# Kernel optimization log

Hardware: AMD Instinct MI355X
Metric: run time of the kernel (lower is better)

Reference implementation:

```python
import jax, jax.numpy as jnp
import numpy as np

# init hyperparameters (from init_kwargs)
KD = KH = KW = 3
SD = SH = SW = 1
PD = PH = PW = 1
DD = DH = DW = 1
GROUPS = 1
DG = 1  # deformable_groups
CIN, COUT = 32, 64


def setup_inputs() -> dict:
    key = jax.random.key(0)
    k1, k2, k3, k4, k5 = jax.random.split(key, 5)
    B, D, H, W = 2, 8, 48, 48
    K = KD * KH * KW
    x = jax.random.normal(k1, (B, CIN, D, H, W), dtype=jnp.float32)
    # 2 offset components (h, w) per deformable-group kernel tap
    offset = jax.random.normal(k2, (B, 2 * DG * K, D, H, W), dtype=jnp.float32)
    mask = jax.random.uniform(k3, (B, DG * K, D, H, W), dtype=jnp.float32)
    fan_in = CIN // GROUPS * K
    weight = jax.random.normal(k4, (COUT, CIN // GROUPS, KD, KH, KW), dtype=jnp.float32) / np.sqrt(fan_in)
    bias = jax.random.uniform(k5, (COUT,), dtype=jnp.float32, minval=-1.0, maxval=1.0) / np.sqrt(fan_in)
    return {"input": x, "offset": offset, "mask": mask, "weight": weight, "bias": bias}


def reference(input, offset, mask, weight, bias):
    x = input
    B, Cin, D, H, W = x.shape
    Cout = weight.shape[0]
    K = KD * KH * KW
    Do = (D + 2 * PD - DD * (KD - 1) - 1) // SD + 1
    Ho = (H + 2 * PH - DH * (KH - 1) - 1) // SH + 1
    Wo = (W + 2 * PW - DW * (KW - 1) - 1) // SW + 1
    Cg = Cin // DG

    kdi, khi, kwi = [a.reshape(-1) for a in jnp.meshgrid(
        jnp.arange(KD), jnp.arange(KH), jnp.arange(KW), indexing="ij")]
    # depth taps: regular (un-deformed) dilated grid -> exact integer index
    d_pos = kdi[:, None] * DD + jnp.arange(Do) * SD - PD           # [K, Do]
    valid_d = (d_pos >= 0) & (d_pos < D)
    d_idx = jnp.clip(d_pos, 0, D - 1)
    h_base = (khi[:, None] * DH + jnp.arange(Ho) * SH - PH).astype(x.dtype)  # [K, Ho]
    w_base = (kwi[:, None] * DW + jnp.arange(Wo) * SW - PW).astype(x.dtype)  # [K, Wo]

    off = offset.reshape(B, DG, K, 2, Do, Ho, Wo)
    m = mask.reshape(B, DG, K, Do, Ho, Wo)

    h = h_base[None, None, :, None, :, None] + off[:, :, :, 0]     # [B,DG,K,Do,Ho,Wo]
    w = w_base[None, None, :, None, None, :] + off[:, :, :, 1]
    h0f, w0f = jnp.floor(h), jnp.floor(w)
    lh, lw = h - h0f, w - w0f
    h0, w0 = h0f.astype(jnp.int32), w0f.astype(jnp.int32)
    h1, w1 = h0 + 1, w0 + 1

    vd = valid_d[None, None, :, :, None, None]
    inb_h = lambda hi: (hi >= 0) & (hi < H)
    inb_w = lambda wi: (wi >= 0) & (wi < W)

    xg = x.reshape(B, DG, Cg, D, H, W)

    def gather(hI, wI):
        hc = jnp.clip(hI, 0, H - 1)
        wc = jnp.clip(wI, 0, W - 1)
        def per(xi, hh, ww):  # xi [Cg,D,H,W]; hh,ww [K,Do,Ho,Wo]
            dfull = jnp.broadcast_to(d_idx[:, :, None, None], hh.shape)
            return xi[:, dfull, hh, ww]  # [Cg,K,Do,Ho,Wo]
        return jax.vmap(jax.vmap(per))(xg, hc, wc)  # [B,DG,Cg,K,Do,Ho,Wo]

    w00 = ((1 - lh) * (1 - lw) * (inb_h(h0) & inb_w(w0) & vd))[:, :, None]
    w01 = ((1 - lh) * lw * (inb_h(h0) & inb_w(w1) & vd))[:, :, None]
    w10 = (lh * (1 - lw) * (inb_h(h1) & inb_w(w0) & vd))[:, :, None]
    w11 = (lh * lw * (inb_h(h1) & inb_w(w1) & vd))[:, :, None]

    val = (gather(h0, w0) * w00 + gather(h0, w1) * w01 +
           gather(h1, w0) * w10 + gather(h1, w1) * w11)   # [B,DG,Cg,K,Do,Ho,Wo]

    sampled = (val * m[:, :, None]).reshape(B, Cin, K, Do, Ho, Wo)
    w2 = weight.reshape(Cout, Cin // GROUPS, K)  # groups == 1
    out = jnp.einsum("bckdhw,ock->bodhw", sampled, w2)
    return out + bias[None, :, None, None, None]
```

## Files before the change

kernel.cpp:

```cpp
#include <hip/hip_runtime.h>
#include <hip/hip_fp16.h>

#define BSZ 2
#define CIN 32
#define COUT 64
#define DD_ 8
#define HH_ 48
#define WW_ 48
#define KK 27
#define HWs (HH_*WW_)
#define DHW (DD_*HH_*WW_)
#define NBLK (BSZ*DD_*HH_)

typedef __attribute__((ext_vector_type(8))) _Float16 half8;
typedef __attribute__((ext_vector_type(4))) float f32x4;

__device__ __forceinline__ half8 splat_h(unsigned packed, int hi) {
    union { unsigned v; _Float16 h[2]; } c; c.v = packed;
    _Float16 e = c.h[hi];
    return (half8){e, e, e, e, e, e, e, e};
}

__global__ void prep(const float* __restrict__ x, const float* __restrict__ wsrc,
                     _Float16* __restrict__ xT, _Float16* __restrict__ wf) {
    __shared__ float tile[CIN][WW_];
    int blk = blockIdx.x;
    if (blk < NBLK) {
        int h = blk % HH_;
        int t0 = blk / HH_;
        int d = t0 % DD_;
        int b = t0 / DD_;
        int base = d * HWs + h * WW_;
        for (int e = threadIdx.x; e < CIN * WW_; e += 256) {
            int ci = e / WW_, w = e - ci * WW_;
            tile[ci][w] = x[(size_t)(b * CIN + ci) * DHW + base + w];
        }
        __syncthreads();
        for (int e = threadIdx.x; e < CIN * WW_; e += 256) {
            int w = e >> 5, ci = e & 31;
            xT[(size_t)(b * DHW + base + w) * CIN + ci] = (_Float16)tile[ci][w];
        }
    } else {
        int idx = (blk - NBLK) * 256 + threadIdx.x;
        if (idx < KK * 4 * 64 * 8) {
            int j = idx & 7, l = (idx >> 3) & 63, c = (idx >> 9) & 3, k = idx >> 11;
            int co = c * 16 + (l & 15), ci = (l >> 4) * 8 + j;
            wf[idx] = (_Float16)wsrc[(co * CIN + ci) * KK + k];
        }
    }
}

__launch_bounds__(192, 3)
__global__ void dcn3d(const _Float16* __restrict__ xT,
                      const float* __restrict__ off, const float* __restrict__ msk,
                      const _Float16* __restrict__ wf,
                      const float* __restrict__ bias, float* __restrict__ out) {
    int blk = blockIdx.x;
    int h = blk % HH_;
    int t0 = blk / HH_;
    int d = t0 % DD_;
    int b = t0 / DD_;

    __shared__ uint4 Pp[KK * WW_];

    int tid = threadIdx.x;
    int lane = tid & 63;
    int T = tid >> 6;
    int wl = lane & 15;
    int g = lane >> 4;
    int spb = d * HWs + h * WW_;

    for (int p = tid; p < KK * WW_; p += 192) {
        int k = p / WW_;
        int w = p - k * WW_;
        int kd = k / 9, kh2 = (k / 3) % 3, kw2 = k % 3;
        int dpos = d + kd - 1;
        bool vd = (dpos >= 0) && (dpos < DD_);
        int didx = min(max(dpos, 0), DD_ - 1);
        int rb = didx * HWs;
        int sp = spb + w;
        float oh = off[(b * (2 * KK) + 2 * k) * DHW + sp];
        float ow = off[(b * (2 * KK) + 2 * k + 1) * DHW + sp];
        float m  = msk[(b * KK + k) * DHW + sp];
        float vm = vd ? m : 0.f;
        float hhf = (float)(kh2 + h - 1) + oh;
        float wwf = (float)(kw2 + w - 1) + ow;
        float h0f = floorf(hhf), w0f = floorf(wwf);
        float lh = hhf - h0f, lw = wwf - w0f;
        int h0 = (int)h0f, w0 = (int)w0f, h1 = h0 + 1, w1 = w0 + 1;
        bool ih0 = (h0 >= 0) && (h0 < HH_), ih1 = (h1 >= 0) && (h1 < HH_);
        bool iw0 = (w0 >= 0) && (w0 < WW_), iw1 = (w1 >= 0) && (w1 < WW_);
        int h0c = min(max(h0, 0), HH_ - 1), h1c = min(max(h1, 0), HH_ - 1);
        int w0c = min(max(w0, 0), WW_ - 1), w1c = min(max(w1, 0), WW_ - 1);
        float f00 = (ih0 && iw0) ? (1.f - lh) * (1.f - lw) * vm : 0.f;
        float f01 = (ih0 && iw1) ? (1.f - lh) * lw * vm : 0.f;
        float f10 = (ih1 && iw0) ? lh * (1.f - lw) * vm : 0.f;
        float f11 = (ih1 && iw1) ? lh * lw * vm : 0.f;
        uint4 P;
        P.x = (unsigned)(rb + h0c * WW_ + w0c) | ((unsigned)(rb + h0c * WW_ + w1c) << 16);
        P.y = (unsigned)(rb + h1c * WW_ + w0c) | ((unsigned)(rb + h1c * WW_ + w1c) << 16);
        __half2 ha = __floats2half2_rn(f00, f01);
        __half2 hb = __floats2half2_rn(f10, f11);
        P.z = *(const unsigned*)&ha;
        P.w = *(const unsigned*)&hb;
        Pp[p] = P;
    }
    __syncthreads();

    const _Float16* bp = xT + (size_t)b * DHW * CIN + g * 8;
    int pbase = T * 16 + wl;

    f32x4 acc0 = {0.f, 0.f, 0.f, 0.f};
    f32x4 acc1 = acc0, acc2 = acc0, acc3 = acc0;

    uint4 P0, P1, P2;
    half8 c0_00, c0_01, c0_10, c0_11;
    half8 c1_00, c1_01, c1_10, c1_11;
    half8 c2_00, c2_01, c2_10, c2_11;

#define PREAD(S, K) P##S = Pp[(K) * WW_ + pbase];
#define CISSUE(S) { \
    c##S##_00 = *(const half8*)(bp + ((size_t)(P##S.x & 0xFFFFu) << 5)); \
    c##S##_01 = *(const half8*)(bp + ((size_t)(P##S.x >> 16) << 5)); \
    c##S##_10 = *(const half8*)(bp + ((size_t)(P##S.y & 0xFFFFu) << 5)); \
    c##S##_11 = *(const half8*)(bp + ((size_t)(P##S.y >> 16) << 5)); }
#define COMP(S, K) { \
    const _Float16* wp = wf + (size_t)(K) * 2048 + lane * 8; \
    half8 a0 = *(const half8*)(wp); \
    half8 a1 = *(const half8*)(wp + 512); \
    half8 a2 = *(const half8*)(wp + 1024); \
    half8 a3 = *(const half8*)(wp + 1536); \
    half8 bf = c##S##_00 * splat_h(P##S.z, 0) + c##S##_01 * splat_h(P##S.z, 1) \
             + c##S##_10 * splat_h(P##S.w, 0) + c##S##_11 * splat_h(P##S.w, 1); \
    acc0 = __builtin_amdgcn_mfma_f32_16x16x32_f16(a0, bf, acc0, 0, 0, 0); \
    acc1 = __builtin_amdgcn_mfma_f32_16x16x32_f16(a1, bf, acc1, 0, 0, 0); \
    acc2 = __builtin_amdgcn_mfma_f32_16x16x32_f16(a2, bf, acc2, 0, 0, 0); \
    acc3 = __builtin_amdgcn_mfma_f32_16x16x32_f16(a3, bf, acc3, 0, 0, 0); }
#define STEP(J, CUR, NX2) CISSUE(NX2) COMP(CUR, J) PREAD(CUR, (J) + 3)

    PREAD(0, 0) PREAD(1, 1) PREAD(2, 2)
    CISSUE(0) CISSUE(1)

    STEP(0, 0, 2)  STEP(1, 1, 0)  STEP(2, 2, 1)
    STEP(3, 0, 2)  STEP(4, 1, 0)  STEP(5, 2, 1)
    STEP(6, 0, 2)  STEP(7, 1, 0)  STEP(8, 2, 1)
    STEP(9, 0, 2)  STEP(10, 1, 0) STEP(11, 2, 1)
    STEP(12, 0, 2) STEP(13, 1, 0) STEP(14, 2, 1)
    STEP(15, 0, 2) STEP(16, 1, 0) STEP(17, 2, 1)
    STEP(18, 0, 2) STEP(19, 1, 0) STEP(20, 2, 1)
    STEP(21, 0, 2) STEP(22, 1, 0) STEP(23, 2, 1)
    CISSUE(2) COMP(0, 24)
    COMP(1, 25)
    COMP(2, 26)

#undef PREAD
#undef CISSUE
#undef COMP
#undef STEP

    int rg = (lane >> 4) * 4;
    int wcol = T * 16 + (lane & 15);
    int obase = (b * COUT * DD_ + d) * HWs + h * WW_ + wcol;
#define ST(C, ACC)                                                         \
    _Pragma("unroll")                                                      \
    for (int r = 0; r < 4; ++r)                                            \
        out[obase + ((C) * 16 + rg + r) * DHW] = ACC[r] + bias[(C) * 16 + rg + r];
    ST(0, acc0) ST(1, acc1) ST(2, acc2) ST(3, acc3)
#undef ST
}

__global__ void dcn3d_ref(const float* __restrict__ x, const float* __restrict__ off,
                          const float* __restrict__ msk, const float* __restrict__ w,
                          const float* __restrict__ bias, float* __restrict__ out) {
    int blk = blockIdx.x;
    int h = blk % HH_;
    int t0 = blk / HH_;
    int d = t0 % DD_;
    int b = t0 / DD_;
    for (int e = threadIdx.x; e < COUT * WW_; e += 256) {
        int co = e / WW_, wo = e - co * WW_;
        float acc = bias[co];
        for (int k = 0; k < KK; ++k) {
            int kd = k / 9, kh2 = (k / 3) % 3, kw2 = k % 3;
            int dpos = d + kd - 1;
            if (dpos < 0 || dpos >= DD_) continue;
            int sp = d * HWs + h * WW_ + wo;
            float oh = off[(b * (2 * KK) + 2 * k) * DHW + sp];
            float ow = off[(b * (2 * KK) + 2 * k + 1) * DHW + sp];
            float m  = msk[(b * KK + k) * DHW + sp];
            float hhf = (float)(kh2 + h - 1) + oh;
            float wwf = (float)(kw2 + wo - 1) + ow;
            float h0f = floorf(hhf), w0f = floorf(wwf);
            float lh = hhf - h0f, lw = wwf - w0f;
            int h0 = (int)h0f, w0 = (int)w0f, h1 = h0 + 1, w1 = w0 + 1;
            bool ih0 = (h0 >= 0) && (h0 < HH_), ih1 = (h1 >= 0) && (h1 < HH_);
            bool iw0 = (w0 >= 0) && (w0 < WW_), iw1 = (w1 >= 0) && (w1 < WW_);
            int h0c = min(max(h0, 0), HH_ - 1), h1c = min(max(h1, 0), HH_ - 1);
            int w0c = min(max(w0, 0), WW_ - 1), w1c = min(max(w1, 0), WW_ - 1);
            float f00 = (ih0 && iw0) ? (1.f - lh) * (1.f - lw) * m : 0.f;
            float f01 = (ih0 && iw1) ? (1.f - lh) * lw * m : 0.f;
            float f10 = (ih1 && iw0) ? lh * (1.f - lw) * m : 0.f;
            float f11 = (ih1 && iw1) ? lh * lw * m : 0.f;
            int rb = dpos * HWs;
            for (int ci = 0; ci < CIN; ++ci) {
                const float* xp = x + (size_t)(b * CIN + ci) * DHW;
                float v = f00 * xp[rb + h0c * WW_ + w0c] + f01 * xp[rb + h0c * WW_ + w1c]
                        + f10 * xp[rb + h1c * WW_ + w0c] + f11 * xp[rb + h1c * WW_ + w1c];
                acc += w[(co * CIN + ci) * KK + k] * v;
            }
        }
        out[((b * COUT + co) * DD_ + d) * HWs + h * WW_ + wo] = acc;
    }
}

extern "C" void kernel_launch(void* const* d_in, const int* in_sizes, int n_in,
                              void* d_out, int out_size, void* d_ws, size_t ws_size,
                              hipStream_t stream) {
    const float* x    = (const float*)d_in[0];
    const float* off  = (const float*)d_in[1];
    const float* msk  = (const float*)d_in[2];
    const float* w    = (const float*)d_in[3];
    const float* bias = (const float*)d_in[4];
    float* out = (float*)d_out;

    const size_t XT_OFF   = 131072;
    const size_t XT_BYTES = (size_t)BSZ * DHW * CIN * sizeof(_Float16);

    _Float16* wf = (_Float16*)d_ws;
    _Float16* xT = (_Float16*)((char*)d_ws + XT_OFF);
    int use = (ws_size >= XT_OFF + XT_BYTES) ? 1 : 0;

    if (use) {
        int wblocks = (KK * 4 * 64 * 8 + 255) / 256;
        prep<<<NBLK + wblocks, 256, 0, stream>>>(x, w, xT, wf);
        dcn3d<<<NBLK, 192, 0, stream>>>(xT, off, msk, wf, bias, out);
    } else {
        dcn3d_ref<<<NBLK, 256, 0, stream>>>(x, off, msk, w, bias, out);
    }
}
```

Before: 42.76 us.

## Split kernel taps across waves with LDS atomic reduction and triple block count

Each block now handles 16 output columns instead of 48, and its four waves split the 27 kernel taps (padded to 28 with zero weights) rather than splitting the output columns. Partial MFMA accumulators are summed through shared-memory atomics before the store. This triples the grid and shortens each wave's serial tap chain to raise occupancy and hide gather latency. In exchange it adds LDS atomic traffic, an extra barrier, and a zero-padded tap.

```diff
diff --git a/kernel.cpp b/kernel.cpp
--- a/kernel.cpp
+++ b/kernel.cpp
@@ -11,6 +11,7 @@
 #define HWs (HH_*WW_)
 #define DHW (DD_*HH_*WW_)
 #define NBLK (BSZ*DD_*HH_)
+#define NTH 256
 
 typedef __attribute__((ext_vector_type(8))) _Float16 half8;
 typedef __attribute__((ext_vector_type(4))) float f32x4;
@@ -42,131 +43,146 @@
         }
     } else {
         int idx = (blk - NBLK) * 256 + threadIdx.x;
-        if (idx < KK * 4 * 64 * 8) {
+        if (idx < 28 * 4 * 64 * 8) {
             int j = idx & 7, l = (idx >> 3) & 63, c = (idx >> 9) & 3, k = idx >> 11;
             int co = c * 16 + (l & 15), ci = (l >> 4) * 8 + j;
-            wf[idx] = (_Float16)wsrc[(co * CIN + ci) * KK + k];
-        }
-    }
-}
-
-__launch_bounds__(192, 3)
+            wf[idx] = (k < KK) ? (_Float16)wsrc[(co * CIN + ci) * KK + k] : (_Float16)0.f;
+        }
+    }
+}
+
+__launch_bounds__(NTH, 5)
 __global__ void dcn3d(const _Float16* __restrict__ xT,
                       const float* __restrict__ off, const float* __restrict__ msk,
                       const _Float16* __restrict__ wf,
                       const float* __restrict__ bias, float* __restrict__ out) {
     int blk = blockIdx.x;
-    int h = blk % HH_;
-    int t0 = blk / HH_;
+    int T = blk % 3;
+    int row = blk / 3;
+    int h = row % HH_;
+    int t0 = row / HH_;
     int d = t0 % DD_;
     int b = t0 / DD_;
-
-    __shared__ uint4 Pp[KK * WW_];
+    int T16 = T * 16;
+
+    __shared__ uint4 Pp[28 * 16];
+    __shared__ float Cred[COUT * 17];
 
     int tid = threadIdx.x;
     int lane = tid & 63;
-    int T = tid >> 6;
+    int q = tid >> 6;
     int wl = lane & 15;
     int g = lane >> 4;
     int spb = d * HWs + h * WW_;
 
-    for (int p = tid; p < KK * WW_; p += 192) {
-        int k = p / WW_;
-        int w = p - k * WW_;
-        int kd = k / 9, kh2 = (k / 3) % 3, kw2 = k % 3;
-        int dpos = d + kd - 1;
-        bool vd = (dpos >= 0) && (dpos < DD_);
-        int didx = min(max(dpos, 0), DD_ - 1);
-        int rb = didx * HWs;
-        int sp = spb + w;
-        float oh = off[(b * (2 * KK) + 2 * k) * DHW + sp];
-        float ow = off[(b * (2 * KK) + 2 * k + 1) * DHW + sp];
-        float m  = msk[(b * KK + k) * DHW + sp];
-        float vm = vd ? m : 0.f;
-        float hhf = (float)(kh2 + h - 1) + oh;
-        float wwf = (float)(kw2 + w - 1) + ow;
-        float h0f = floorf(hhf), w0f = floorf(wwf);
-        float lh = hhf - h0f, lw = wwf - w0f;
-        int h0 = (int)h0f, w0 = (int)w0f, h1 = h0 + 1, w1 = w0 + 1;
-        bool ih0 = (h0 >= 0) && (h0 < HH_), ih1 = (h1 >= 0) && (h1 < HH_);
-        bool iw0 = (w0 >= 0) && (w0 < WW_), iw1 = (w1 >= 0) && (w1 < WW_);
-        int h0c = min(max(h0, 0), HH_ - 1), h1c = min(max(h1, 0), HH_ - 1);
-        int w0c = min(max(w0, 0), WW_ - 1), w1c = min(max(w1, 0), WW_ - 1);
-        float f00 = (ih0 && iw0) ? (1.f - lh) * (1.f - lw) * vm : 0.f;
-        float f01 = (ih0 && iw1) ? (1.f - lh) * lw * vm : 0.f;
-        float f10 = (ih1 && iw0) ? lh * (1.f - lw) * vm : 0.f;
-        float f11 = (ih1 && iw1) ? lh * lw * vm : 0.f;
-        uint4 P;
-        P.x = (unsigned)(rb + h0c * WW_ + w0c) | ((unsigned)(rb + h0c * WW_ + w1c) << 16);
-        P.y = (unsigned)(rb + h1c * WW_ + w0c) | ((unsigned)(rb + h1c * WW_ + w1c) << 16);
-        __half2 ha = __floats2half2_rn(f00, f01);
-        __half2 hb = __floats2half2_rn(f10, f11);
-        P.z = *(const unsigned*)&ha;
-        P.w = *(const unsigned*)&hb;
-        Pp[p] = P;
-    }
+    for (int e = tid; e < COUT * 17; e += NTH) Cred[e] = 0.f;
+
+#define PARAM(PIDX)                                                            \
+    {                                                                          \
+        int p = (PIDX);                                                        \
+        int k = p >> 4;                                                        \
+        uint4 P;                                                               \
+        if (k < KK) {                                                          \
+            int w = T16 + (p & 15);                                            \
+            int kd = k / 9, kh2 = (k / 3) % 3, kw2 = k % 3;                    \
+            int dpos = d + kd - 1;                                             \
+            bool vd = (dpos >= 0) && (dpos < DD_);                             \
+            int didx = min(max(dpos, 0), DD_ - 1);                             \
+            int rb = didx * HWs;                                               \
+            int sp = spb + w;                                                  \
+            float oh = off[(b * (2 * KK) + 2 * k) * DHW + sp];                 \
+            float ow = off[(b * (2 * KK) + 2 * k + 1) * DHW + sp];             \
+            float m  = msk[(b * KK + k) * DHW + sp];                           \
+            float vm = vd ? m : 0.f;                                           \
+            float hhf = (float)(kh2 + h - 1) + oh;                             \
+            float wwf = (float)(kw2 + w - 1) + ow;                             \
+            float h0f = floorf(hhf), w0f = floorf(wwf);                        \
+            float lh = hhf - h0f, lw = wwf - w0f;                              \
+            int h0 = (int)h0f, w0 = (int)w0f, h1 = h0 + 1, w1 = w0 + 1;        \
+            bool ih0 = (h0 >= 0) && (h0 < HH_), ih1 = (h1 >= 0) && (h1 < HH_); \
+            bool iw0 = (w0 >= 0) && (w0 < WW_), iw1 = (w1 >= 0) && (w1 < WW_); \
+            int h0c = min(max(h0, 0), HH_ - 1), h1c = min(max(h1, 0), HH_ - 1);\
+            int w0c = min(max(w0, 0), WW_ - 1), w1c = min(max(w1, 0), WW_ - 1);\
+            float f00 = (ih0 && iw0) ? (1.f - lh) * (1.f - lw) * vm : 0.f;     \
+            float f01 = (ih0 && iw1) ? (1.f - lh) * lw * vm : 0.f;             \
+            float f10 = (ih1 && iw0) ? lh * (1.f - lw) * vm : 0.f;             \
+            float f11 = (ih1 && iw1) ? lh * lw * vm : 0.f;                     \
+            P.x = (unsigned)(rb + h0c * WW_ + w0c)                             \
+                | ((unsigned)(rb + h0c * WW_ + w1c) << 16);                    \
+            P.y = (unsigned)(rb + h1c * WW_ + w0c)                             \
+                | ((unsigned)(rb + h1c * WW_ + w1c) << 16);                    \
+            __half2 ha = __floats2half2_rn(f00, f01);                          \
+            __half2 hb = __floats2half2_rn(f10, f11);                          \
+            P.z = *(const unsigned*)&ha;                                       \
+            P.w = *(const unsigned*)&hb;                                       \
+        } else {                                                               \
+            P.x = 0u; P.y = 0u; P.z = 0u; P.w = 0u;                            \
+        }                                                                      \
+        Pp[p] = P;                                                             \
+    }
+
+    PARAM(tid)
+    if (tid < 192) PARAM(tid + 256)
+#undef PARAM
     __syncthreads();
 
     const _Float16* bp = xT + (size_t)b * DHW * CIN + g * 8;
-    int pbase = T * 16 + wl;
 
     f32x4 acc0 = {0.f, 0.f, 0.f, 0.f};
     f32x4 acc1 = acc0, acc2 = acc0, acc3 = acc0;
 
-    uint4 P0, P1, P2;
-    half8 c0_00, c0_01, c0_10, c0_11;
-    half8 c1_00, c1_01, c1_10, c1_11;
-    half8 c2_00, c2_01, c2_10, c2_11;
-
-#define PREAD(S, K) P##S = Pp[(K) * WW_ + pbase];
-#define CISSUE(S) { \
-    c##S##_00 = *(const half8*)(bp + ((size_t)(P##S.x & 0xFFFFu) << 5)); \
-    c##S##_01 = *(const half8*)(bp + ((size_t)(P##S.x >> 16) << 5)); \
-    c##S##_10 = *(const half8*)(bp + ((size_t)(P##S.y & 0xFFFFu) << 5)); \
-    c##S##_11 = *(const half8*)(bp + ((size_t)(P##S.y >> 16) << 5)); }
-#define COMP(S, K) { \
-    const _Float16* wp = wf + (size_t)(K) * 2048 + lane * 8; \
+    uint4 PA, PB;
+    int kA, kB;
+    half8 cA00, cA01, cA10, cA11;
+    half8 cB00, cB01, cB10, cB11;
+
+#define PRD(S, I) { k##S = q + 4 * (I); P##S = Pp[(k##S << 4) + wl]; }
+#define ISS(S) { \
+    c##S##00 = *(const half8*)(bp + ((size_t)(P##S.x & 0xFFFFu) << 5)); \
+    c##S##01 = *(const half8*)(bp + ((size_t)(P##S.x >> 16) << 5)); \
+    c##S##10 = *(const half8*)(bp + ((size_t)(P##S.y & 0xFFFFu) << 5)); \
+    c##S##11 = *(const half8*)(bp + ((size_t)(P##S.y >> 16) << 5)); }
+#define CMP(S) { \
+    const _Float16* wp = wf + (size_t)k##S * 2048 + lane * 8; \
     half8 a0 = *(const half8*)(wp); \
     half8 a1 = *(const half8*)(wp + 512); \
     half8 a2 = *(const half8*)(wp + 1024); \
     half8 a3 = *(const half8*)(wp + 1536); \
-    half8 bf = c##S##_00 * splat_h(P##S.z, 0) + c##S##_01 * splat_h(P##S.z, 1) \
-             + c##S##_10 * splat_h(P##S.w, 0) + c##S##_11 * splat_h(P##S.w, 1); \
+    half8 bf = c##S##00 * splat_h(P##S.z, 0) + c##S##01 * splat_h(P##S.z, 1) \
+             + c##S##10 * splat_h(P##S.w, 0) + c##S##11 * splat_h(P##S.w, 1); \
     acc0 = __builtin_amdgcn_mfma_f32_16x16x32_f16(a0, bf, acc0, 0, 0, 0); \
     acc1 = __builtin_amdgcn_mfma_f32_16x16x32_f16(a1, bf, acc1, 0, 0, 0); \
     acc2 = __builtin_amdgcn_mfma_f32_16x16x32_f16(a2, bf, acc2, 0, 0, 0); \
     acc3 = __builtin_amdgcn_mfma_f32_16x16x32_f16(a3, bf, acc3, 0, 0, 0); }
-#define STEP(J, CUR, NX2) CISSUE(NX2) COMP(CUR, J) PREAD(CUR, (J) + 3)
-
-    PREAD(0, 0) PREAD(1, 1) PREAD(2, 2)
-    CISSUE(0) CISSUE(1)
-
-    STEP(0, 0, 2)  STEP(1, 1, 0)  STEP(2, 2, 1)
-    STEP(3, 0, 2)  STEP(4, 1, 0)  STEP(5, 2, 1)
-    STEP(6, 0, 2)  STEP(7, 1, 0)  STEP(8, 2, 1)
-    STEP(9, 0, 2)  STEP(10, 1, 0) STEP(11, 2, 1)
-    STEP(12, 0, 2) STEP(13, 1, 0) STEP(14, 2, 1)
-    STEP(15, 0, 2) STEP(16, 1, 0) STEP(17, 2, 1)
-    STEP(18, 0, 2) STEP(19, 1, 0) STEP(20, 2, 1)
-    STEP(21, 0, 2) STEP(22, 1, 0) STEP(23, 2, 1)
-    CISSUE(2) COMP(0, 24)
-    COMP(1, 25)
-    COMP(2, 26)
-
-#undef PREAD
-#undef CISSUE
-#undef COMP
-#undef STEP
-
-    int rg = (lane >> 4) * 4;
-    int wcol = T * 16 + (lane & 15);
-    int obase = (b * COUT * DD_ + d) * HWs + h * WW_ + wcol;
-#define ST(C, ACC)                                                         \
-    _Pragma("unroll")                                                      \
-    for (int r = 0; r < 4; ++r)                                            \
-        out[obase + ((C) * 16 + rg + r) * DHW] = ACC[r] + bias[(C) * 16 + rg + r];
-    ST(0, acc0) ST(1, acc1) ST(2, acc2) ST(3, acc3)
-#undef ST
+
+    PRD(A, 0) ISS(A)
+    PRD(B, 1) ISS(B)
+    CMP(A) PRD(A, 2) ISS(A)
+    CMP(B) PRD(B, 3) ISS(B)
+    CMP(A) PRD(A, 4) ISS(A)
+    CMP(B) PRD(B, 5) ISS(B)
+    CMP(A) PRD(A, 6) ISS(A)
+    CMP(B)
+    CMP(A)
+
+#undef PRD
+#undef ISS
+#undef CMP
+
+    int rg = g * 4;
+#define RED(C, ACC)                                                            \
+    _Pragma("unroll")                                                          \
+    for (int r = 0; r < 4; ++r)                                                \
+        atomicAdd(&Cred[((C) * 16 + rg + r) * 17 + wl], ACC[r]);
+    RED(0, acc0) RED(1, acc1) RED(2, acc2) RED(3, acc3)
+#undef RED
+    __syncthreads();
+
+    for (int e = tid; e < COUT * 16; e += NTH) {
+        int co = e >> 4, w = e & 15;
+        out[((b * COUT + co) * DD_ + d) * HWs + h * WW_ + T16 + w]
+            = Cred[co * 17 + w] + bias[co];
+    }
 }
 
 __global__ void dcn3d_ref(const float* __restrict__ x, const float* __restrict__ off,
@@ -231,9 +247,9 @@
     int use = (ws_size >= XT_OFF + XT_BYTES) ? 1 : 0;
 
     if (use) {
-        int wblocks = (KK * 4 * 64 * 8 + 255) / 256;
+        int wblocks = (28 * 4 * 64 * 8 + 255) / 256;
         prep<<<NBLK + wblocks, 256, 0, stream>>>(x, w, xT, wf);
-        dcn3d<<<NBLK, 192, 0, stream>>>(xT, off, msk, wf, bias, out);
+        dcn3d<<<NBLK * 3, NTH, 0, stream>>>(xT, off, msk, wf, bias, out);
     } else {
         dcn3d_ref<<<NBLK, 256, 0, stream>>>(x, off, msk, w, bias, out);
     }
```

New measurement: 83.26 us. +94.7%, slower.
